# Kernel optimization log

Measured on AMD Instinct MI355X. Metric: run time of the kernel, lower is better.

## Reference

```python
import jax, jax.numpy as jnp
import numpy as np

B, H, S, D = 4, 16, 2048, 64
INV_SCALE_FACTOR = 8.0  # scores are divided by this (== sqrt(D))
DROPOUT_P = 0.0         # deterministic baseline; dropout is identity at p=0


def setup_inputs() -> dict:
    key = jax.random.key(0)
    kq, kk, kv = jax.random.split(key, 3)
    return {
        "query": jax.random.normal(kq, (B, H, S, D), dtype=jnp.float32),
        "key": jax.random.normal(kk, (B, H, S, D), dtype=jnp.float32),
        "value": jax.random.normal(kv, (B, H, S, D), dtype=jnp.float32),
    }


def reference(query, key, value):
    # scores: [B, H, Sq, Sk]
    scores = jnp.einsum("bhqd,bhkd->bhqk", query, key) / INV_SCALE_FACTOR
    probs = jax.nn.softmax(scores, axis=-1)
    # dropout_p == 0.0 -> identity
    out = jnp.einsum("bhqk,bhkd->bhqd", probs, value)
    return out
```

## Files before the change

### kernel.cpp

```cpp
#include <hip/hip_runtime.h>


#define S_LEN 2048
#define D_DIM 64
#define TK    128
#define NTILE (S_LEN / TK)
#define LOG2E_OVER8 0.18033688011112042f

typedef __bf16 bf16x8 __attribute__((ext_vector_type(8)));
typedef __bf16 bf16x4 __attribute__((ext_vector_type(4)));
typedef short  s16x4  __attribute__((ext_vector_type(4)));
typedef float  f32x4  __attribute__((ext_vector_type(4)));
typedef unsigned short us4 __attribute__((ext_vector_type(4)));
typedef unsigned short us;

__device__ __forceinline__ us f2bf(float f) {
    union { __bf16 h; us u; } c;
    c.h = (__bf16)f;
    return c.u;
}

__device__ __forceinline__ void gload_lds16(const void* g, void* l) {
    __builtin_amdgcn_global_load_lds(
        (const __attribute__((address_space(1))) unsigned int*)g,
        (__attribute__((address_space(3))) unsigned int*)l, 16, 0, 0);
}

__device__ __forceinline__ f32x4 mfma16x16x16(s16x4 a, s16x4 b, f32x4 c) {
#if __has_builtin(__builtin_amdgcn_mfma_f32_16x16x16bf16_1k)
    return __builtin_amdgcn_mfma_f32_16x16x16bf16_1k(a, b, c, 0, 0, 0);
#else
    f32x4 d = c;
    asm volatile("v_mfma_f32_16x16x16_bf16 %0, %1, %2, %0"
                 : "+v"(d) : "v"(a), "v"(b));
    return d;
#endif
}

__global__ __launch_bounds__(256)
void prep(const float* __restrict__ Q, const float* __restrict__ K,
          const float* __restrict__ V, us* __restrict__ Qb,
          us* __restrict__ Kb, us* __restrict__ Vt) {
    __shared__ float Lt[64 * 68];
    const int bx = blockIdx.x, tid = threadIdx.x;
    if (bx < 8192) {
        const bool isQ = bx < 4096;
        const size_t i = ((size_t)(isQ ? bx : bx - 4096) * 256 + tid) * 8;
        const float* src = (isQ ? Q : K) + i;
        us* dst = (isQ ? Qb : Kb) + i;
        const float s = isQ ? LOG2E_OVER8 : 1.0f;
        const float4 a = *(const float4*)src;
        const float4 b = *(const float4*)(src + 4);
        union { us u[8]; uint4 q; } pk;
        pk.u[0] = f2bf(a.x * s); pk.u[1] = f2bf(a.y * s);
        pk.u[2] = f2bf(a.z * s); pk.u[3] = f2bf(a.w * s);
        pk.u[4] = f2bf(b.x * s); pk.u[5] = f2bf(b.y * s);
        pk.u[6] = f2bf(b.z * s); pk.u[7] = f2bf(b.w * s);
        *(uint4*)dst = pk.q;
    } else {
        const int idx = bx - 8192;
        const int t = idx & 31, bh = idx >> 5;
        {
            const int sl = tid >> 2, dc = (tid & 3) * 16;
            const float* src = V + ((size_t)bh * S_LEN + t * 64 + sl) * D_DIM + dc;
#pragma unroll
            for (int i = 0; i < 4; ++i)
                *(float4*)&Lt[sl * 68 + dc + 4 * i] = *(const float4*)(src + 4 * i);
        }
        __syncthreads();
        {
            const int d = tid >> 2, s0 = (tid & 3) * 16;
            union { us u[16]; uint4 q[2]; } pk;
#pragma unroll
            for (int j = 0; j < 16; ++j) pk.u[j] = f2bf(Lt[(s0 + j) * 68 + d]);
            us* dst = Vt + ((size_t)bh * 64 + d) * S_LEN + t * 64 + s0;
            *(uint4*)dst = pk.q[0];
            *(uint4*)(dst + 8) = pk.q[1];
        }
    }
}

__global__ __launch_bounds__(256, 4)
void fa_fwd(const us* __restrict__ Qb, const us* __restrict__ Kb,
            const us* __restrict__ Vtb, float* __restrict__ Og) {
    __shared__ __align__(16) us Kl[TK * 64];
    __shared__ __align__(16) us Vl[64 * TK];

    const int tid  = threadIdx.x;
    const int w    = tid >> 6;
    const int lane = tid & 63;
    const int l15  = lane & 15;
    const int quad = lane >> 4;
    const int bh = blockIdx.y, qb = blockIdx.x;
    const size_t base = (size_t)bh * S_LEN * D_DIM;

    const us* qp = Qb + base + (size_t)(qb * 64 + w * 16 + l15) * D_DIM + quad * 8;
    const bf16x8 bq0 = *(const bf16x8*)qp;
    const bf16x8 bq1 = *(const bf16x8*)(qp + 32);

    const int krow = w * 32 + (lane >> 3);
    const int kchunk = (lane & 7) ^ (lane >> 3);
    const us* ksrc = Kb + base + (size_t)krow * D_DIM + kchunk * 8;
    const us* vsrc[4];
#pragma unroll
    for (int j = 0; j < 4; ++j) {
        const int vrow = w * 16 + j * 4 + (lane >> 4);
        const int vchunk = (lane & 15) ^ (j * 4 + (lane >> 4));
        vsrc[j] = Vtb + (size_t)bh * 64 * S_LEN + (size_t)vrow * S_LEN + vchunk * 8;
    }
    us* kld = &Kl[w * 2048];
    us* vld = &Vl[w * 2048];

    float l_q = 0.f;
    f32x4 oa[4];
#pragma unroll
    for (int db = 0; db < 4; ++db) oa[db] = (f32x4){0.f, 0.f, 0.f, 0.f};

#pragma unroll 1
    for (int t = 0; t < NTILE; ++t) {
        __syncthreads();
#pragma unroll
        for (int j = 0; j < 4; ++j)
            gload_lds16(ksrc + (size_t)t * (TK * D_DIM) + j * 512, kld + j * 512);
#pragma unroll
        for (int j = 0; j < 4; ++j)
            gload_lds16(vsrc[j] + t * TK, vld + j * 512);
        __syncthreads();

        bf16x4 pb[8];
#pragma unroll
        for (int kb = 0; kb < 8; ++kb) {
            const int row = kb * 16 + l15;
            const int x = l15 & 7;
            const bf16x8 a0 = *(const bf16x8*)&Kl[row * 64 + ((quad ^ x) * 8)];
            const bf16x8 a1 = *(const bf16x8*)&Kl[row * 64 + (((4 + quad) ^ x) * 8)];
            f32x4 c = {0.f, 0.f, 0.f, 0.f};
            c = __builtin_amdgcn_mfma_f32_16x16x32_bf16(a0, bq0, c, 0, 0, 0);
            c = __builtin_amdgcn_mfma_f32_16x16x32_bf16(a1, bq1, c, 0, 0, 0);
#pragma unroll
            for (int r = 0; r < 4; ++r) {
                const float p = exp2f(c[r]);
                l_q += p;
                pb[kb][r] = (__bf16)p;
            }
        }

#pragma unroll
        for (int kb = 0; kb < 8; ++kb) {
            union { bf16x4 h; s16x4 s; } bu;
            bu.h = pb[kb];
            const int vcol = (((kb * 2 + (quad >> 1)) ^ l15) * 8) + (quad & 1) * 4;
#pragma unroll
            for (int db = 0; db < 4; ++db) {
                union { bf16x4 h; s16x4 s; } au;
                au.h = *(const bf16x4*)&Vl[(db * 16 + l15) * TK + vcol];
                oa[db] = mfma16x16x16(au.s, bu.s, oa[db]);
            }
        }
    }

    l_q += __shfl_xor(l_q, 16, 64);
    l_q += __shfl_xor(l_q, 32, 64);
    const float inv = 1.f / l_q;
    float* op = Og + base + (size_t)(qb * 64 + w * 16 + l15) * D_DIM + quad * 4;
#pragma unroll
    for (int db = 0; db < 4; ++db) {
        float4 v = { oa[db][0] * inv, oa[db][1] * inv, oa[db][2] * inv, oa[db][3] * inv };
        *(float4*)(op + db * 16) = v;
    }
}

extern "C" void kernel_launch(void* const* d_in, const int* in_sizes, int n_in,
                              void* d_out, int out_size, void* d_ws, size_t ws_size,
                              hipStream_t stream) {
    const float* Q = (const float*)d_in[0];
    const float* K = (const float*)d_in[1];
    const float* V = (const float*)d_in[2];
    float* O = (float*)d_out;

    us* Qb = (us*)d_ws;
    us* Kb = Qb + (size_t)64 * S_LEN * D_DIM;
    us* Vt = Kb + (size_t)64 * S_LEN * D_DIM;

    prep<<<10240, 256, 0, stream>>>(Q, K, V, Qb, Kb, Vt);
    fa_fwd<<<dim3(32, 64), 256, 0, stream>>>(Qb, Kb, Vt, O);
}
```

Before: 248.5 us.

## Fuse Q conversion into attention kernel and pad V tile layout

Removes the Q bf16 pre-conversion pass, so the attention kernel now loads fp32 Q, scales it and converts it in registers. V is transposed in 128-row tiles into a padded per-tile layout (row stride 136), which allows linear global-to-LDS copies and unswizzled LDS reads. The exp/PV loops are merged so P is consumed per kb block, using hardware exp2, packed bf16 conversion and a vector row-sum accumulator. The trade-offs are a larger Vt workspace with padding, an extra partial load by wave 0, and possible LDS bank conflicts from the padded stride.

Measured after the change: 231.4 us. 6.9% less time.

```diff
diff --git a/kernel.cpp b/kernel.cpp
--- a/kernel.cpp
+++ b/kernel.cpp
@@ -6,6 +6,9 @@
 #define TK    128
 #define NTILE (S_LEN / TK)
 #define LOG2E_OVER8 0.18033688011112042f
+#define VROW  136
+#define VTILE (64 * VROW)
+#define VBH   (NTILE * VTILE)
 
 typedef __bf16 bf16x8 __attribute__((ext_vector_type(8)));
 typedef __bf16 bf16x4 __attribute__((ext_vector_type(4)));
@@ -18,6 +21,25 @@
     union { __bf16 h; us u; } c;
     c.h = (__bf16)f;
     return c.u;
+}
+
+__device__ __forceinline__ unsigned pk2(float a, float b) {
+#if __has_builtin(__builtin_amdgcn_cvt_pk_bf16_f32)
+    typedef __bf16 bf2 __attribute__((ext_vector_type(2)));
+    union { bf2 h; unsigned u; } c;
+    c.h = __builtin_amdgcn_cvt_pk_bf16_f32(a, b);
+    return c.u;
+#else
+    return ((unsigned)f2bf(b) << 16) | f2bf(a);
+#endif
+}
+
+__device__ __forceinline__ float fast_exp2(float x) {
+#if __has_builtin(__builtin_amdgcn_exp2f)
+    return __builtin_amdgcn_exp2f(x);
+#else
+    return exp2f(x);
+#endif
 }
 
 __device__ __forceinline__ void gload_lds16(const void* g, void* l) {
@@ -38,80 +60,92 @@
 }
 
 __global__ __launch_bounds__(256)
-void prep(const float* __restrict__ Q, const float* __restrict__ K,
-          const float* __restrict__ V, us* __restrict__ Qb,
+void prep(const float* __restrict__ K, const float* __restrict__ V,
           us* __restrict__ Kb, us* __restrict__ Vt) {
-    __shared__ float Lt[64 * 68];
+    __shared__ us Ls[128 * 68];
     const int bx = blockIdx.x, tid = threadIdx.x;
-    if (bx < 8192) {
-        const bool isQ = bx < 4096;
-        const size_t i = ((size_t)(isQ ? bx : bx - 4096) * 256 + tid) * 8;
-        const float* src = (isQ ? Q : K) + i;
-        us* dst = (isQ ? Qb : Kb) + i;
-        const float s = isQ ? LOG2E_OVER8 : 1.0f;
-        const float4 a = *(const float4*)src;
-        const float4 b = *(const float4*)(src + 4);
+    if (bx < 4096) {
+        const size_t i = ((size_t)bx * 256 + tid) * 8;
+        const float4 a = *(const float4*)(K + i);
+        const float4 b = *(const float4*)(K + i + 4);
         union { us u[8]; uint4 q; } pk;
-        pk.u[0] = f2bf(a.x * s); pk.u[1] = f2bf(a.y * s);
-        pk.u[2] = f2bf(a.z * s); pk.u[3] = f2bf(a.w * s);
-        pk.u[4] = f2bf(b.x * s); pk.u[5] = f2bf(b.y * s);
-        pk.u[6] = f2bf(b.z * s); pk.u[7] = f2bf(b.w * s);
-        *(uint4*)dst = pk.q;
+        pk.u[0] = f2bf(a.x); pk.u[1] = f2bf(a.y);
+        pk.u[2] = f2bf(a.z); pk.u[3] = f2bf(a.w);
+        pk.u[4] = f2bf(b.x); pk.u[5] = f2bf(b.y);
+        pk.u[6] = f2bf(b.z); pk.u[7] = f2bf(b.w);
+        *(uint4*)(Kb + i) = pk.q;
     } else {
-        const int idx = bx - 8192;
-        const int t = idx & 31, bh = idx >> 5;
+        const int idx = bx - 4096;
+        const int t = idx & (NTILE - 1), bh = idx >> 4;
         {
-            const int sl = tid >> 2, dc = (tid & 3) * 16;
-            const float* src = V + ((size_t)bh * S_LEN + t * 64 + sl) * D_DIM + dc;
-#pragma unroll
-            for (int i = 0; i < 4; ++i)
-                *(float4*)&Lt[sl * 68 + dc + 4 * i] = *(const float4*)(src + 4 * i);
+            const int r = tid >> 1, h = tid & 1;
+            const float* src = V + ((size_t)bh * S_LEN + t * TK + r) * D_DIM + h * 32;
+            us* dst = &Ls[r * 68 + h * 32];
+#pragma unroll
+            for (int i = 0; i < 4; ++i) {
+                const float4 v0 = *(const float4*)(src + 8 * i);
+                const float4 v1 = *(const float4*)(src + 8 * i + 4);
+                union { us u[8]; uint2 q[2]; } pk;
+                pk.u[0] = f2bf(v0.x); pk.u[1] = f2bf(v0.y);
+                pk.u[2] = f2bf(v0.z); pk.u[3] = f2bf(v0.w);
+                pk.u[4] = f2bf(v1.x); pk.u[5] = f2bf(v1.y);
+                pk.u[6] = f2bf(v1.z); pk.u[7] = f2bf(v1.w);
+                *(uint2*)(dst + 8 * i) = pk.q[0];
+                *(uint2*)(dst + 8 * i + 4) = pk.q[1];
+            }
         }
         __syncthreads();
         {
-            const int d = tid >> 2, s0 = (tid & 3) * 16;
-            union { us u[16]; uint4 q[2]; } pk;
-#pragma unroll
-            for (int j = 0; j < 16; ++j) pk.u[j] = f2bf(Lt[(s0 + j) * 68 + d]);
-            us* dst = Vt + ((size_t)bh * 64 + d) * S_LEN + t * 64 + s0;
-            *(uint4*)dst = pk.q[0];
-            *(uint4*)(dst + 8) = pk.q[1];
+            const int d = tid >> 2, sc = tid & 3;
+            union { us u[32]; uint4 q[4]; } pk;
+#pragma unroll
+            for (int j = 0; j < 32; ++j) pk.u[j] = Ls[(sc * 32 + j) * 68 + d];
+            us* dst = Vt + (size_t)bh * VBH + t * VTILE + d * VROW + sc * 32;
+#pragma unroll
+            for (int i = 0; i < 4; ++i) *(uint4*)(dst + 8 * i) = pk.q[i];
         }
     }
 }
 
 __global__ __launch_bounds__(256, 4)
-void fa_fwd(const us* __restrict__ Qb, const us* __restrict__ Kb,
+void fa_fwd(const float* __restrict__ Qg, const us* __restrict__ Kb,
             const us* __restrict__ Vtb, float* __restrict__ Og) {
     __shared__ __align__(16) us Kl[TK * 64];
-    __shared__ __align__(16) us Vl[64 * TK];
+    __shared__ __align__(16) us Vl[64 * VROW];
 
     const int tid  = threadIdx.x;
     const int w    = tid >> 6;
     const int lane = tid & 63;
     const int l15  = lane & 15;
     const int quad = lane >> 4;
+    const int x    = l15 & 7;
     const int bh = blockIdx.y, qb = blockIdx.x;
     const size_t base = (size_t)bh * S_LEN * D_DIM;
 
-    const us* qp = Qb + base + (size_t)(qb * 64 + w * 16 + l15) * D_DIM + quad * 8;
-    const bf16x8 bq0 = *(const bf16x8*)qp;
-    const bf16x8 bq1 = *(const bf16x8*)(qp + 32);
+    bf16x8 bq0, bq1;
+    {
+        const float* qrow = Qg + base + (size_t)(qb * 64 + w * 16 + l15) * D_DIM + quad * 8;
+        const float4 x0 = *(const float4*)qrow;
+        const float4 x1 = *(const float4*)(qrow + 4);
+        const float4 y0 = *(const float4*)(qrow + 32);
+        const float4 y1 = *(const float4*)(qrow + 36);
+        bq0[0]=(__bf16)(x0.x*LOG2E_OVER8); bq0[1]=(__bf16)(x0.y*LOG2E_OVER8);
+        bq0[2]=(__bf16)(x0.z*LOG2E_OVER8); bq0[3]=(__bf16)(x0.w*LOG2E_OVER8);
+        bq0[4]=(__bf16)(x1.x*LOG2E_OVER8); bq0[5]=(__bf16)(x1.y*LOG2E_OVER8);
+        bq0[6]=(__bf16)(x1.z*LOG2E_OVER8); bq0[7]=(__bf16)(x1.w*LOG2E_OVER8);
+        bq1[0]=(__bf16)(y0.x*LOG2E_OVER8); bq1[1]=(__bf16)(y0.y*LOG2E_OVER8);
+        bq1[2]=(__bf16)(y0.z*LOG2E_OVER8); bq1[3]=(__bf16)(y0.w*LOG2E_OVER8);
+        bq1[4]=(__bf16)(y1.x*LOG2E_OVER8); bq1[5]=(__bf16)(y1.y*LOG2E_OVER8);
+        bq1[6]=(__bf16)(y1.z*LOG2E_OVER8); bq1[7]=(__bf16)(y1.w*LOG2E_OVER8);
+    }
 
     const int krow = w * 32 + (lane >> 3);
     const int kchunk = (lane & 7) ^ (lane >> 3);
     const us* ksrc = Kb + base + (size_t)krow * D_DIM + kchunk * 8;
-    const us* vsrc[4];
-#pragma unroll
-    for (int j = 0; j < 4; ++j) {
-        const int vrow = w * 16 + j * 4 + (lane >> 4);
-        const int vchunk = (lane & 15) ^ (j * 4 + (lane >> 4));
-        vsrc[j] = Vtb + (size_t)bh * 64 * S_LEN + (size_t)vrow * S_LEN + vchunk * 8;
-    }
     us* kld = &Kl[w * 2048];
-    us* vld = &Vl[w * 2048];
-
-    float l_q = 0.f;
+    const us* vlane = Vtb + (size_t)bh * VBH + lane * 8;
+
+    f32x4 lv = {0.f, 0.f, 0.f, 0.f};
     f32x4 oa[4];
 #pragma unroll
     for (int db = 0; db < 4; ++db) oa[db] = (f32x4){0.f, 0.f, 0.f, 0.f};
@@ -122,43 +156,41 @@
 #pragma unroll
         for (int j = 0; j < 4; ++j)
             gload_lds16(ksrc + (size_t)t * (TK * D_DIM) + j * 512, kld + j * 512);
+        const us* vt = vlane + (size_t)t * VTILE;
 #pragma unroll
         for (int j = 0; j < 4; ++j)
-            gload_lds16(vsrc[j] + t * TK, vld + j * 512);
+            gload_lds16(vt + (w * 4 + j) * 512, Vl + (w * 4 + j) * 512);
+        if (w == 0) gload_lds16(vt + 16 * 512, Vl + 16 * 512);
         __syncthreads();
 
-        bf16x4 pb[8];
 #pragma unroll
         for (int kb = 0; kb < 8; ++kb) {
             const int row = kb * 16 + l15;
-            const int x = l15 & 7;
             const bf16x8 a0 = *(const bf16x8*)&Kl[row * 64 + ((quad ^ x) * 8)];
             const bf16x8 a1 = *(const bf16x8*)&Kl[row * 64 + (((4 + quad) ^ x) * 8)];
             f32x4 c = {0.f, 0.f, 0.f, 0.f};
             c = __builtin_amdgcn_mfma_f32_16x16x32_bf16(a0, bq0, c, 0, 0, 0);
             c = __builtin_amdgcn_mfma_f32_16x16x32_bf16(a1, bq1, c, 0, 0, 0);
-#pragma unroll
-            for (int r = 0; r < 4; ++r) {
-                const float p = exp2f(c[r]);
-                l_q += p;
-                pb[kb][r] = (__bf16)p;
-            }
-        }
-
-#pragma unroll
-        for (int kb = 0; kb < 8; ++kb) {
-            union { bf16x4 h; s16x4 s; } bu;
-            bu.h = pb[kb];
-            const int vcol = (((kb * 2 + (quad >> 1)) ^ l15) * 8) + (quad & 1) * 4;
+
+            const float p0 = fast_exp2(c[0]);
+            const float p1 = fast_exp2(c[1]);
+            const float p2 = fast_exp2(c[2]);
+            const float p3 = fast_exp2(c[3]);
+            lv += (f32x4){p0, p1, p2, p3};
+            union { unsigned u[2]; s16x4 s; } bu;
+            bu.u[0] = pk2(p0, p1);
+            bu.u[1] = pk2(p2, p3);
+
 #pragma unroll
             for (int db = 0; db < 4; ++db) {
                 union { bf16x4 h; s16x4 s; } au;
-                au.h = *(const bf16x4*)&Vl[(db * 16 + l15) * TK + vcol];
+                au.h = *(const bf16x4*)&Vl[l15 * VROW + quad * 4 + db * (16 * VROW) + kb * 16];
                 oa[db] = mfma16x16x16(au.s, bu.s, oa[db]);
             }
         }
     }
 
+    float l_q = lv[0] + lv[1] + lv[2] + lv[3];
     l_q += __shfl_xor(l_q, 16, 64);
     l_q += __shfl_xor(l_q, 32, 64);
     const float inv = 1.f / l_q;
@@ -178,10 +210,9 @@
     const float* V = (const float*)d_in[2];
     float* O = (float*)d_out;
 
-    us* Qb = (us*)d_ws;
-    us* Kb = Qb + (size_t)64 * S_LEN * D_DIM;
+    us* Kb = (us*)d_ws;
     us* Vt = Kb + (size_t)64 * S_LEN * D_DIM;
 
-    prep<<<10240, 256, 0, stream>>>(Q, K, V, Qb, Kb, Vt);
-    fa_fwd<<<dim3(32, 64), 256, 0, stream>>>(Qb, Kb, Vt, O);
-}
+    prep<<<4096 + 1024, 256, 0, stream>>>(K, V, Kb, Vt);
+    fa_fwd<<<dim3(32, 64), 256, 0, stream>>>(Q, Kb, Vt, O);
+}
```
